# Kernel tuning notes

Measured on AMD Instinct MI355X. Metric: run time of the kernel, lower is better.

Reference implementation:

```python
import jax, jax.numpy as jnp
import numpy as np

IN_FEATURES = 4096
OUT_FEATURES = 4096
BANDWIDTH = min(IN_FEATURES, OUT_FEATURES) // 8  # 512, as in the torch default


def band_indices(n_out, n_in, bw):
    """Vectorized equivalent of BandMatrix.create_band_indices (COO row/col lists)."""
    i = np.arange(n_out)
    lo = np.maximum(0, i - bw)
    hi = np.minimum(n_in, i + bw + 1)
    counts = hi - lo
    total = int(counts.sum())
    rows = np.repeat(i, counts)
    start = np.cumsum(counts) - counts  # offset of each row's first entry
    cols = np.arange(total) - np.repeat(start, counts) + np.repeat(lo, counts)
    return rows.astype(np.int32), cols.astype(np.int32)


def setup_inputs() -> dict:
    key = jax.random.key(0)
    kx, kw = jax.random.split(key)
    rows_np, cols_np = band_indices(OUT_FEATURES, IN_FEATURES, BANDWIDTH)
    nnz = rows_np.shape[0]  # 3935744
    x = jax.random.normal(kx, (4, 2048, IN_FEATURES), dtype=jnp.float32)
    W_values = jax.random.normal(kw, (nnz,), dtype=jnp.float32)
    bias = jnp.zeros((OUT_FEATURES,), dtype=jnp.float32)
    return {
        "x": x,
        "W_values": W_values,
        "bias": bias,
        "rows": jnp.asarray(rows_np),
        "cols": jnp.asarray(cols_np),
    }


def reference(x, W_values, bias, rows, cols):
    # Densify banded COO weight [out, in] (matches sparse_coo_tensor().to_dense()).
    W = jnp.zeros((OUT_FEATURES, IN_FEATURES), dtype=W_values.dtype).at[rows, cols].set(W_values)
    # x: [B, S, in] @ W.T: [in, out] -> [B, S, out]
    out = jnp.einsum('bsi,oi->bso', x, W) + bias
    return out
```

## Files before the change

kernel.cpp:

```cpp
#include <hip/hip_runtime.h>
#include <stdint.h>

#define IN_F  4096
#define OUT_F 4096
#define BW    512
#define WB2   1280
#define BM    256
#define BN    256

typedef __bf16 bf16x8 __attribute__((ext_vector_type(8)));
typedef float  f32x4  __attribute__((ext_vector_type(4)));

__device__ __forceinline__ int band_start(int o) {
    if (o <= 512)  return o * 513 + ((o * (o - 1)) >> 1);
    if (o <= 3584) return 393472 + (o - 512) * 1025;
    const int d = o - 3584;
    return 3542272 + (((1024 + 4609 - o) * d) >> 1);
}

__device__ __forceinline__ uint16_t f32_to_bf16(float f) {
    uint32_t u = __builtin_bit_cast(uint32_t, f);
    u += 0x7FFFu + ((u >> 16) & 1u);
    return (uint16_t)(u >> 16);
}

__global__ __launch_bounds__(256) void cvt_x(const float* __restrict__ x,
                                             uint16_t* __restrict__ xb, int n4) {
    const int stride = gridDim.x * 256;
    for (int i = blockIdx.x * 256 + threadIdx.x; i < n4; i += stride) {
        const float4 v = reinterpret_cast<const float4*>(x)[i];
        const uint32_t lo = (uint32_t)f32_to_bf16(v.x) | ((uint32_t)f32_to_bf16(v.y) << 16);
        const uint32_t hi = (uint32_t)f32_to_bf16(v.z) | ((uint32_t)f32_to_bf16(v.w) << 16);
        reinterpret_cast<uint2*>(xb)[i] = make_uint2(lo, hi);
    }
}

__global__ __launch_bounds__(256) void cvt_w(const float* __restrict__ wv,
                                             uint16_t* __restrict__ wd) {
    const int o = blockIdx.y;
    const int j = blockIdx.x * 256 + threadIdx.x;
    const int i = (o & ~(BM - 1)) - BW + j;
    uint16_t v = 0;
    if (i >= o - BW && i <= o + BW && i >= 0 && i < IN_F) {
        const int lo = (o > BW) ? (o - BW) : 0;
        v = f32_to_bf16(wv[band_start(o) + (i - lo)]);
    }
    wd[o * WB2 + j] = v;
}

__global__ __launch_bounds__(512, 1) void band_gemm_v5(
    const uint16_t* __restrict__ xb,
    const uint16_t* __restrict__ wd,
    const float* __restrict__ bias,
    float* __restrict__ out)
{
    __shared__ __align__(128) uint8_t lds[131072];

    const int id  = blockIdx.x;
    const int xcd = id & 7;
    const int r   = id >> 3;
    const int bx  = 2 * xcd + (r & 1);
    const int by  = r >> 1;
    const int brow = by * BM;
    const int bcol = bx * BN;

    const int wlo    = bcol - BW;
    const int kstart = wlo > 0 ? wlo : 0;
    const int kend   = (bcol + BN + BW) < IN_F ? (bcol + BN + BW) : IN_F;
    const int nt     = (kend - kstart) >> 6;
    const int j0     = kstart - wlo;

    const int tid  = threadIdx.x;
    const int w    = tid >> 6;
    const int lane = tid & 63;
    const int ln   = lane & 15;
    const int kc   = lane >> 4;
    const int wm   = w >> 2;
    const int wn   = w & 3;

    const int srow = tid >> 3;
    const int csrc = (tid & 7) ^ (srow & 7);
    const uint16_t* aSrc = xb + (size_t)(brow + srow) * IN_F + kstart + csrc * 8;
    const uint16_t* bSrc = wd + (size_t)(bcol + srow) * WB2 + j0 + csrc * 8;

#define GLOAD(srcp, dst_off)                                                             \
    __builtin_amdgcn_global_load_lds(                                                    \
        (const __attribute__((address_space(1))) uint32_t*)(srcp),                       \
        (__attribute__((address_space(3))) uint32_t*)(lds + (dst_off) + (w << 10)),      \
        16, 0, 0)

#define STAGE(ts_, sb_) {                                                                \
        const uint16_t* as_ = aSrc + (ts_) * 64;                                         \
        const uint16_t* bs_ = bSrc + (ts_) * 64;                                         \
        GLOAD(as_,                        (sb_) + 0);                                    \
        GLOAD(as_ + (size_t)64  * IN_F,   (sb_) + 8192);                                 \
        GLOAD(as_ + (size_t)128 * IN_F,   (sb_) + 16384);                                \
        GLOAD(as_ + (size_t)192 * IN_F,   (sb_) + 24576);                                \
        GLOAD(bs_,                        (sb_) + 32768);                                 \
        GLOAD(bs_ + (size_t)64  * WB2,    (sb_) + 40960);                                \
        GLOAD(bs_ + (size_t)128 * WB2,    (sb_) + 49152);                                \
        GLOAD(bs_ + (size_t)192 * WB2,    (sb_) + 57344); }

    const int cswz = (kc ^ (ln & 7)) << 4;
    int aOff[8], bOff[4];
    #pragma unroll
    for (int a = 0; a < 8; ++a) aOff[a] = ((wm * 128 + a * 16 + ln) << 7) + cswz;
    #pragma unroll
    for (int n = 0; n < 4; ++n) bOff[n] = 32768 + ((wn * 64 + n * 16 + ln) << 7) + cswz;

    f32x4 acc[8][4] = {};

    STAGE(0, 0);
    asm volatile("s_waitcnt vmcnt(0)" ::: "memory");
    __builtin_amdgcn_s_barrier();

    for (int t = 0; t < nt; ++t) {
        const int cur = (t & 1) << 16;

        if (t + 1 < nt) STAGE(t + 1, cur ^ 65536);

        bf16x8 bfr[4][2];
        #pragma unroll
        for (int n = 0; n < 4; ++n) {
            bfr[n][0] = *(const bf16x8*)(lds + cur + bOff[n]);
            bfr[n][1] = *(const bf16x8*)(lds + cur + (bOff[n] ^ 64));
        }

        #pragma unroll
        for (int mq = 0; mq < 2; ++mq) {
            bf16x8 af[4][2];
            #pragma unroll
            for (int a = 0; a < 4; ++a) {
                af[a][0] = *(const bf16x8*)(lds + cur + aOff[mq * 4 + a]);
                af[a][1] = *(const bf16x8*)(lds + cur + (aOff[mq * 4 + a] ^ 64));
            }
            __builtin_amdgcn_s_setprio(1);
            #pragma unroll
            for (int a = 0; a < 4; ++a)
                #pragma unroll
                for (int n = 0; n < 4; ++n) {
                    acc[mq * 4 + a][n] = __builtin_amdgcn_mfma_f32_16x16x32_bf16(
                        af[a][0], bfr[n][0], acc[mq * 4 + a][n], 0, 0, 0);
                    acc[mq * 4 + a][n] = __builtin_amdgcn_mfma_f32_16x16x32_bf16(
                        af[a][1], bfr[n][1], acc[mq * 4 + a][n], 0, 0, 0);
                }
            __builtin_amdgcn_s_setprio(0);
        }

        asm volatile("s_waitcnt vmcnt(0)" ::: "memory");
        __builtin_amdgcn_s_barrier();
    }
#undef STAGE
#undef GLOAD

    const int ocol = bcol + wn * 64 + ln;
    float bsv[4];
    #pragma unroll
    for (int n = 0; n < 4; ++n) bsv[n] = bias[ocol + n * 16];

    #pragma unroll
    for (int a = 0; a < 8; ++a) {
        #pragma unroll
        for (int q = 0; q < 4; ++q) {
            const int row = brow + wm * 128 + a * 16 + (kc << 2) + q;
            float* po = out + (size_t)row * OUT_F + ocol;
            #pragma unroll
            for (int n = 0; n < 4; ++n)
                po[n * 16] = acc[a][n][q] + bsv[n];
        }
    }
}

__global__ __launch_bounds__(256) void band_gemm_f32(
    const float* __restrict__ x, const float* __restrict__ wv,
    const float* __restrict__ bias, float* __restrict__ out, int M)
{
    __shared__ float Xs[128][33];
    __shared__ float Ws[32][130];
    const int tid = threadIdx.x;
    const int tx = tid & 15, ty = tid >> 4;
    const int bcol = blockIdx.x * 128, brow = blockIdx.y * 128;
    const int klo = (bcol >= BW) ? (bcol - BW) : 0;
    const int khi = min(IN_F, bcol + 128 + BW);
    float acc[8][8];
    #pragma unroll
    for (int a = 0; a < 8; ++a)
        #pragma unroll
        for (int b = 0; b < 8; ++b) acc[a][b] = 0.f;
    const int xc4 = (tid & 7) * 4, xr0 = tid >> 3;
    const int wc = tid & 31, wr0 = tid >> 5;
    for (int k0 = klo; k0 < khi; k0 += 32) {
        #pragma unroll
        for (int p = 0; p < 4; ++p) {
            const int r = xr0 + 32 * p;
            const float4 v = *reinterpret_cast<const float4*>(&x[(size_t)(brow + r) * IN_F + (k0 + xc4)]);
            Xs[r][xc4 + 0] = v.x; Xs[r][xc4 + 1] = v.y; Xs[r][xc4 + 2] = v.z; Xs[r][xc4 + 3] = v.w;
        }
        const int i = k0 + wc;
        #pragma unroll
        for (int p = 0; p < 16; ++p) {
            const int rr = wr0 + 8 * p;
            const int o = bcol + rr;
            const int lo = (o >= BW) ? (o - BW) : 0;
            float v = 0.f;
            if (i >= o - BW && i <= o + BW) v = wv[band_start(o) + (i - lo)];
            Ws[wc][rr] = v;
        }
        __syncthreads();
        #pragma unroll
        for (int k = 0; k < 32; ++k) {
            float am[8];
            #pragma unroll
            for (int a = 0; a < 8; ++a) am[a] = Xs[ty * 8 + a][k];
            float bo[8];
            #pragma unroll
            for (int b = 0; b < 4; ++b) { bo[b] = Ws[k][tx * 4 + b]; bo[4 + b] = Ws[k][tx * 4 + 64 + b]; }
            #pragma unroll
            for (int a = 0; a < 8; ++a)
                #pragma unroll
                for (int b = 0; b < 8; ++b) acc[a][b] = fmaf(am[a], bo[b], acc[a][b]);
        }
        __syncthreads();
    }
    #pragma unroll
    for (int a = 0; a < 8; ++a) {
        const size_t row = (size_t)(brow + ty * 8 + a);
        #pragma unroll
        for (int b = 0; b < 4; ++b) {
            out[row * OUT_F + bcol + tx * 4 + b]      = acc[a][b]     + bias[bcol + tx * 4 + b];
            out[row * OUT_F + bcol + tx * 4 + 64 + b] = acc[a][4 + b] + bias[bcol + tx * 4 + 64 + b];
        }
    }
}

extern "C" void kernel_launch(void* const* d_in, const int* in_sizes, int n_in,
                              void* d_out, int out_size, void* d_ws, size_t ws_size,
                              hipStream_t stream) {
    const float* x    = (const float*)d_in[0];
    const float* wv   = (const float*)d_in[1];
    const float* bias = (const float*)d_in[2];
    float* out        = (float*)d_out;

    const int M = in_sizes[0] / IN_F;
    const size_t xb_bytes = (size_t)M * IN_F * 2;
    const size_t wd_bytes = (size_t)OUT_F * WB2 * 2;

    if (ws_size >= xb_bytes + wd_bytes && (M % BM) == 0) {
        uint16_t* xb  = (uint16_t*)d_ws;
        uint16_t* wdp = (uint16_t*)((uint8_t*)d_ws + xb_bytes);
        cvt_x<<<2048, 256, 0, stream>>>(x, xb, M * IN_F / 4);
        cvt_w<<<dim3(WB2 / 256, OUT_F), 256, 0, stream>>>(wv, wdp);
        band_gemm_v5<<<(M / BM) * (OUT_F / BN), 512, 0, stream>>>(xb, wdp, bias, out);
    } else {
        dim3 grid(OUT_F / 128, M / 128);
        band_gemm_f32<<<grid, 256, 0, stream>>>(x, wv, bias, out, M);
    }
}
```

Baseline: 140.7 us.

## Restructure band GEMM main loop into finer-grained phased load/compute pipeline

Replaces the simple double-buffered K loop with a two-tile-unrolled schedule. Each 64-wide K tile is split into A and B halves that are staged independently, interleaved with four MFMA quadrant phases, barriers, and partial vmcnt waits. This lets global-to-LDS loads overlap MFMA work more finely instead of waiting for all loads at the end of each iteration. Launch bounds also change to request 2 blocks per CU. The 128 KB LDS allocation likely keeps occupancy at one block, while the extra register pressure and barriers add risk. The loop assumes an even tile count.

After: 142.5 us. About the same (+1.3%).

```diff
diff --git a/kernel.cpp b/kernel.cpp
--- a/kernel.cpp
+++ b/kernel.cpp
@@ -48,7 +48,7 @@
     wd[o * WB2 + j] = v;
 }
 
-__global__ __launch_bounds__(512, 1) void band_gemm_v5(
+__global__ __launch_bounds__(512, 2) void band_gemm_v6(
     const uint16_t* __restrict__ xb,
     const uint16_t* __restrict__ wd,
     const float* __restrict__ bias,
@@ -68,6 +68,7 @@
     const int kstart = wlo > 0 ? wlo : 0;
     const int kend   = (bcol + BN + BW) < IN_F ? (bcol + BN + BW) : IN_F;
     const int nt     = (kend - kstart) >> 6;
+    const int niter  = nt >> 1;
     const int j0     = kstart - wlo;
 
     const int tid  = threadIdx.x;
@@ -89,68 +90,94 @@
         (__attribute__((address_space(3))) uint32_t*)(lds + (dst_off) + (w << 10)),      \
         16, 0, 0)
 
-#define STAGE(ts_, sb_) {                                                                \
-        const uint16_t* as_ = aSrc + (ts_) * 64;                                         \
-        const uint16_t* bs_ = bSrc + (ts_) * 64;                                         \
-        GLOAD(as_,                        (sb_) + 0);                                    \
-        GLOAD(as_ + (size_t)64  * IN_F,   (sb_) + 8192);                                 \
-        GLOAD(as_ + (size_t)128 * IN_F,   (sb_) + 16384);                                \
-        GLOAD(as_ + (size_t)192 * IN_F,   (sb_) + 24576);                                \
-        GLOAD(bs_,                        (sb_) + 32768);                                 \
-        GLOAD(bs_ + (size_t)64  * WB2,    (sb_) + 40960);                                \
-        GLOAD(bs_ + (size_t)128 * WB2,    (sb_) + 49152);                                \
-        GLOAD(bs_ + (size_t)192 * WB2,    (sb_) + 57344); }
-
-    const int cswz = (kc ^ (ln & 7)) << 4;
-    int aOff[8], bOff[4];
-    #pragma unroll
-    for (int a = 0; a < 8; ++a) aOff[a] = ((wm * 128 + a * 16 + ln) << 7) + cswz;
-    #pragma unroll
-    for (int n = 0; n < 4; ++n) bOff[n] = 32768 + ((wn * 64 + n * 16 + ln) << 7) + cswz;
+#define STG_A(v, h, dst) { const uint16_t* p_ = aSrc + (size_t)((h) * 128) * IN_F + (v) * 64; \
+        GLOAD(p_, dst); GLOAD(p_ + (size_t)64 * IN_F, (dst) + 8192); }
+#define STG_B(v, h, dst) { const uint16_t* p_ = bSrc + (size_t)((h) * 128) * WB2 + (v) * 64;  \
+        GLOAD(p_, dst); GLOAD(p_ + (size_t)64 * WB2, (dst) + 8192); }
+
+    const int cswz     = (kc ^ (ln & 7)) << 4;
+    const int aRowBase = wm * 16384 + (ln << 7);
+    const int bRowBase = (wn >> 1) * 16384 + (((wn & 1) * 64 + ln) << 7);
+
+#define LD_AF(BB, MQ) {                                                                  \
+    _Pragma("unroll")                                                                    \
+    for (int a_ = 0; a_ < 4; ++a_) {                                                     \
+        af[a_][0] = *(const bf16x8*)(lds + (BB) + aRowBase + (MQ) * 8192 + a_ * 2048 + cswz);        \
+        af[a_][1] = *(const bf16x8*)(lds + (BB) + aRowBase + (MQ) * 8192 + a_ * 2048 + (cswz ^ 64)); \
+    } }
+#define LD_BF(BB, NQ, BF) {                                                              \
+    _Pragma("unroll")                                                                    \
+    for (int n_ = 0; n_ < 2; ++n_) {                                                     \
+        BF[n_][0] = *(const bf16x8*)(lds + (BB) + bRowBase + (NQ) * 4096 + n_ * 2048 + cswz);        \
+        BF[n_][1] = *(const bf16x8*)(lds + (BB) + bRowBase + (NQ) * 4096 + n_ * 2048 + (cswz ^ 64)); \
+    } }
+#define MFMA16(MQ, NQ, BF) {                                                             \
+    _Pragma("unroll")                                                                    \
+    for (int a_ = 0; a_ < 4; ++a_) {                                                     \
+        _Pragma("unroll")                                                                \
+        for (int n_ = 0; n_ < 2; ++n_) {                                                 \
+            acc[(MQ)*4+a_][(NQ)*2+n_] = __builtin_amdgcn_mfma_f32_16x16x32_bf16(         \
+                af[a_][0], BF[n_][0], acc[(MQ)*4+a_][(NQ)*2+n_], 0, 0, 0);               \
+            acc[(MQ)*4+a_][(NQ)*2+n_] = __builtin_amdgcn_mfma_f32_16x16x32_bf16(         \
+                af[a_][1], BF[n_][1], acc[(MQ)*4+a_][(NQ)*2+n_], 0, 0, 0);               \
+        } } }
+#define PH_SYNC  __builtin_amdgcn_s_barrier();                                           \
+                 asm volatile("s_waitcnt lgkmcnt(0)" ::: "memory");                      \
+                 __builtin_amdgcn_sched_barrier(0);                                      \
+                 __builtin_amdgcn_s_setprio(1)
+#define PH_END   __builtin_amdgcn_s_setprio(0);                                          \
+                 __builtin_amdgcn_s_barrier()
 
     f32x4 acc[8][4] = {};
 
-    STAGE(0, 0);
-    asm volatile("s_waitcnt vmcnt(0)" ::: "memory");
+    STG_A(0, 0, 0);      STG_A(0, 1, 16384);
+    STG_B(0, 0, 32768);  STG_B(0, 1, 49152);
+    STG_B(1, 0, 98304);  STG_A(1, 0, 65536);
+    asm volatile("s_waitcnt vmcnt(4)" ::: "memory");
     __builtin_amdgcn_s_barrier();
 
-    for (int t = 0; t < nt; ++t) {
-        const int cur = (t & 1) << 16;
-
-        if (t + 1 < nt) STAGE(t + 1, cur ^ 65536);
-
-        bf16x8 bfr[4][2];
-        #pragma unroll
-        for (int n = 0; n < 4; ++n) {
-            bfr[n][0] = *(const bf16x8*)(lds + cur + bOff[n]);
-            bfr[n][1] = *(const bf16x8*)(lds + cur + (bOff[n] ^ 64));
-        }
-
-        #pragma unroll
-        for (int mq = 0; mq < 2; ++mq) {
-            bf16x8 af[4][2];
-            #pragma unroll
-            for (int a = 0; a < 4; ++a) {
-                af[a][0] = *(const bf16x8*)(lds + cur + aOff[mq * 4 + a]);
-                af[a][1] = *(const bf16x8*)(lds + cur + (aOff[mq * 4 + a] ^ 64));
-            }
-            __builtin_amdgcn_s_setprio(1);
-            #pragma unroll
-            for (int a = 0; a < 4; ++a)
-                #pragma unroll
-                for (int n = 0; n < 4; ++n) {
-                    acc[mq * 4 + a][n] = __builtin_amdgcn_mfma_f32_16x16x32_bf16(
-                        af[a][0], bfr[n][0], acc[mq * 4 + a][n], 0, 0, 0);
-                    acc[mq * 4 + a][n] = __builtin_amdgcn_mfma_f32_16x16x32_bf16(
-                        af[a][1], bfr[n][1], acc[mq * 4 + a][n], 0, 0, 0);
-                }
-            __builtin_amdgcn_s_setprio(0);
-        }
-
-        asm volatile("s_waitcnt vmcnt(0)" ::: "memory");
-        __builtin_amdgcn_s_barrier();
-    }
-#undef STAGE
+    for (int t = 0; t < niter; ++t) {
+        const int u   = 2 * t;
+        const bool st = (t + 1 < niter);
+        bf16x8 af[4][2], bf0[2][2], bf1[2][2];
+
+        LD_AF(0, 0); LD_BF(32768, 0, bf0);
+        STG_A(u + 1, 1, 81920);
+        PH_SYNC; MFMA16(0, 0, bf0); PH_END;
+        LD_BF(32768, 1, bf1);
+        STG_B(u + 1, 1, 114688);
+        PH_SYNC; MFMA16(0, 1, bf1); PH_END;
+        LD_AF(0, 1);
+        if (st) STG_B(u + 2, 0, 32768);
+        PH_SYNC; MFMA16(1, 1, bf1); PH_END;
+        if (st) STG_A(u + 2, 0, 0);
+        __builtin_amdgcn_s_barrier();
+        __builtin_amdgcn_s_setprio(1);
+        MFMA16(1, 0, bf0);
+        __builtin_amdgcn_s_setprio(0);
+        if (st) { asm volatile("s_waitcnt vmcnt(4)" ::: "memory"); }
+        else    { asm volatile("s_waitcnt vmcnt(0)" ::: "memory"); }
+        __builtin_amdgcn_s_barrier();
+        LD_AF(65536, 0); LD_BF(98304, 0, bf0);
+        if (st) STG_A(u + 2, 1, 16384);
+        PH_SYNC; MFMA16(0, 0, bf0); PH_END;
+        LD_BF(98304, 1, bf1);
+        if (st) STG_B(u + 2, 1, 49152);
+        PH_SYNC; MFMA16(0, 1, bf1); PH_END;
+        LD_AF(65536, 1);
+        if (st) STG_B(u + 3, 0, 98304);
+        PH_SYNC; MFMA16(1, 1, bf1); PH_END;
+        if (st) STG_A(u + 3, 0, 65536);
+        __builtin_amdgcn_s_barrier();
+        __builtin_amdgcn_s_setprio(1);
+        MFMA16(1, 0, bf0);
+        __builtin_amdgcn_s_setprio(0);
+        if (st) { asm volatile("s_waitcnt vmcnt(4)" ::: "memory"); }
+        else    { asm volatile("s_waitcnt vmcnt(0)" ::: "memory"); }
+        __builtin_amdgcn_s_barrier();
+    }
+#undef STG_A
+#undef STG_B
 #undef GLOAD
 
     const int ocol = bcol + wn * 64 + ln;
@@ -192,9 +219,9 @@
     for (int k0 = klo; k0 < khi; k0 += 32) {
         #pragma unroll
         for (int p = 0; p < 4; ++p) {
-            const int r = xr0 + 32 * p;
-            const float4 v = *reinterpret_cast<const float4*>(&x[(size_t)(brow + r) * IN_F + (k0 + xc4)]);
-            Xs[r][xc4 + 0] = v.x; Xs[r][xc4 + 1] = v.y; Xs[r][xc4 + 2] = v.z; Xs[r][xc4 + 3] = v.w;
+            const int rr = xr0 + 32 * p;
+            const float4 v = *reinterpret_cast<const float4*>(&x[(size_t)(brow + rr) * IN_F + (k0 + xc4)]);
+            Xs[rr][xc4 + 0] = v.x; Xs[rr][xc4 + 1] = v.y; Xs[rr][xc4 + 2] = v.z; Xs[rr][xc4 + 3] = v.w;
         }
         const int i = k0 + wc;
         #pragma unroll
@@ -250,7 +277,7 @@
         uint16_t* wdp = (uint16_t*)((uint8_t*)d_ws + xb_bytes);
         cvt_x<<<2048, 256, 0, stream>>>(x, xb, M * IN_F / 4);
         cvt_w<<<dim3(WB2 / 256, OUT_F), 256, 0, stream>>>(wv, wdp);
-        band_gemm_v5<<<(M / BM) * (OUT_F / BN), 512, 0, stream>>>(xb, wdp, bias, out);
+        band_gemm_v6<<<(M / BM) * (OUT_F / BN), 512, 0, stream>>>(xb, wdp, bias, out);
     } else {
         dim3 grid(OUT_F / 128, M / 128);
         band_gemm_f32<<<grid, 256, 0, stream>>>(x, wv, bias, out, M);
```

## Software-pipeline LDS fragment loads with MFMA quadrants and prefetch two stages ahead

Applied to the files above, without the earlier changes.

Restructures the main loop of the banded bf16 GEMM into a ping-pong schedule. LDS fragment loads for the next quadrant and next tile are interleaved with MFMA blocks, and global-to-LDS staging is issued two tiles ahead instead of one. The goal is to hide LDS read latency and global load latency behind matrix-core work. The cost is more live registers for the double fragment buffers, an extra barrier per iteration, and more intricate synchronisation that could introduce races if the vmcnt and barrier placement is wrong.

Result: no change. 143.1 us (+1.7%).

```diff
diff --git a/kernel.cpp b/kernel.cpp
--- a/kernel.cpp
+++ b/kernel.cpp
@@ -48,7 +48,7 @@
     wd[o * WB2 + j] = v;
 }
 
-__global__ __launch_bounds__(512, 1) void band_gemm_v5(
+__global__ __launch_bounds__(512, 1) void band_gemm_v7(
     const uint16_t* __restrict__ xb,
     const uint16_t* __restrict__ wd,
     const float* __restrict__ bias,
@@ -96,7 +96,7 @@
         GLOAD(as_ + (size_t)64  * IN_F,   (sb_) + 8192);                                 \
         GLOAD(as_ + (size_t)128 * IN_F,   (sb_) + 16384);                                \
         GLOAD(as_ + (size_t)192 * IN_F,   (sb_) + 24576);                                \
-        GLOAD(bs_,                        (sb_) + 32768);                                 \
+        GLOAD(bs_,                        (sb_) + 32768);                                \
         GLOAD(bs_ + (size_t)64  * WB2,    (sb_) + 40960);                                \
         GLOAD(bs_ + (size_t)128 * WB2,    (sb_) + 49152);                                \
         GLOAD(bs_ + (size_t)192 * WB2,    (sb_) + 57344); }
@@ -108,47 +108,62 @@
     #pragma unroll
     for (int n = 0; n < 4; ++n) bOff[n] = 32768 + ((wn * 64 + n * 16 + ln) << 7) + cswz;
 
+    bf16x8 a0[4][2], a1[4][2], b0[2][2], b1[2][2];
+
+#define LD_A(DST, BB, MQ) {                                                              \
+    _Pragma("unroll")                                                                    \
+    for (int a_ = 0; a_ < 4; ++a_) {                                                     \
+        DST[a_][0] = *(const bf16x8*)(lds + (BB) + aOff[(MQ) * 4 + a_]);                 \
+        DST[a_][1] = *(const bf16x8*)(lds + (BB) + (aOff[(MQ) * 4 + a_] ^ 64));          \
+    } }
+#define LD_B(DST, BB, NQ) {                                                              \
+    _Pragma("unroll")                                                                    \
+    for (int n_ = 0; n_ < 2; ++n_) {                                                     \
+        DST[n_][0] = *(const bf16x8*)(lds + (BB) + bOff[(NQ) * 2 + n_]);                 \
+        DST[n_][1] = *(const bf16x8*)(lds + (BB) + (bOff[(NQ) * 2 + n_] ^ 64));          \
+    } }
+#define MFMAQ(AF, BF, MQ, NQ) {                                                          \
+    __builtin_amdgcn_s_setprio(1);                                                       \
+    _Pragma("unroll")                                                                    \
+    for (int a_ = 0; a_ < 4; ++a_) {                                                     \
+        _Pragma("unroll")                                                                \
+        for (int n_ = 0; n_ < 2; ++n_) {                                                 \
+            acc[(MQ)*4+a_][(NQ)*2+n_] = __builtin_amdgcn_mfma_f32_16x16x32_bf16(         \
+                AF[a_][0], BF[n_][0], acc[(MQ)*4+a_][(NQ)*2+n_], 0, 0, 0);               \
+            acc[(MQ)*4+a_][(NQ)*2+n_] = __builtin_amdgcn_mfma_f32_16x16x32_bf16(         \
+                AF[a_][1], BF[n_][1], acc[(MQ)*4+a_][(NQ)*2+n_], 0, 0, 0);               \
+        } }                                                                              \
+    __builtin_amdgcn_s_setprio(0); }
+
     f32x4 acc[8][4] = {};
 
     STAGE(0, 0);
-    asm volatile("s_waitcnt vmcnt(0)" ::: "memory");
+    STAGE(1, 65536);
+    asm volatile("s_waitcnt vmcnt(8)" ::: "memory");
     __builtin_amdgcn_s_barrier();
-
-    for (int t = 0; t < nt; ++t) {
-        const int cur = (t & 1) << 16;
-
-        if (t + 1 < nt) STAGE(t + 1, cur ^ 65536);
-
-        bf16x8 bfr[4][2];
-        #pragma unroll
-        for (int n = 0; n < 4; ++n) {
-            bfr[n][0] = *(const bf16x8*)(lds + cur + bOff[n]);
-            bfr[n][1] = *(const bf16x8*)(lds + cur + (bOff[n] ^ 64));
-        }
-
-        #pragma unroll
-        for (int mq = 0; mq < 2; ++mq) {
-            bf16x8 af[4][2];
-            #pragma unroll
-            for (int a = 0; a < 4; ++a) {
-                af[a][0] = *(const bf16x8*)(lds + cur + aOff[mq * 4 + a]);
-                af[a][1] = *(const bf16x8*)(lds + cur + (aOff[mq * 4 + a] ^ 64));
-            }
-            __builtin_amdgcn_s_setprio(1);
-            #pragma unroll
-            for (int a = 0; a < 4; ++a)
-                #pragma unroll
-                for (int n = 0; n < 4; ++n) {
-                    acc[mq * 4 + a][n] = __builtin_amdgcn_mfma_f32_16x16x32_bf16(
-                        af[a][0], bfr[n][0], acc[mq * 4 + a][n], 0, 0, 0);
-                    acc[mq * 4 + a][n] = __builtin_amdgcn_mfma_f32_16x16x32_bf16(
-                        af[a][1], bfr[n][1], acc[mq * 4 + a][n], 0, 0, 0);
-                }
-            __builtin_amdgcn_s_setprio(0);
-        }
-
+    LD_A(a0, 0, 0);
+    LD_B(b1, 0, 1);
+
+    for (int v = 0; v < nt; ++v) {
+        const int cur = (v & 1) << 16;
+        const int nxt = cur ^ 65536;
+
+        LD_B(b0, cur, 0);
+        LD_A(a1, cur, 1);
+        MFMAQ(a0, b0, 0, 0);
+
+        MFMAQ(a0, b1, 0, 1);
         asm volatile("s_waitcnt vmcnt(0)" ::: "memory");
         __builtin_amdgcn_s_barrier();
+
+        if (v + 1 < nt) LD_A(a0, nxt, 0);
+        MFMAQ(a1, b1, 1, 1);
+        __builtin_amdgcn_s_barrier();
+        __builtin_amdgcn_sched_barrier(0);
+
+        if (v + 2 < nt) STAGE(v + 2, cur);
+        if (v + 1 < nt) LD_B(b1, nxt, 1);
+        MFMAQ(a1, b0, 1, 0);
     }
 #undef STAGE
 #undef GLOAD
@@ -192,9 +207,9 @@
     for (int k0 = klo; k0 < khi; k0 += 32) {
         #pragma unroll
         for (int p = 0; p < 4; ++p) {
-            const int r = xr0 + 32 * p;
-            const float4 v = *reinterpret_cast<const float4*>(&x[(size_t)(brow + r) * IN_F + (k0 + xc4)]);
-            Xs[r][xc4 + 0] = v.x; Xs[r][xc4 + 1] = v.y; Xs[r][xc4 + 2] = v.z; Xs[r][xc4 + 3] = v.w;
+            const int rr = xr0 + 32 * p;
+            const float4 v = *reinterpret_cast<const float4*>(&x[(size_t)(brow + rr) * IN_F + (k0 + xc4)]);
+            Xs[rr][xc4 + 0] = v.x; Xs[rr][xc4 + 1] = v.y; Xs[rr][xc4 + 2] = v.z; Xs[rr][xc4 + 3] = v.w;
         }
         const int i = k0 + wc;
         #pragma unroll
@@ -250,7 +265,7 @@
         uint16_t* wdp = (uint16_t*)((uint8_t*)d_ws + xb_bytes);
         cvt_x<<<2048, 256, 0, stream>>>(x, xb, M * IN_F / 4);
         cvt_w<<<dim3(WB2 / 256, OUT_F), 256, 0, stream>>>(wv, wdp);
-        band_gemm_v5<<<(M / BM) * (OUT_F / BN), 512, 0, stream>>>(xb, wdp, bias, out);
+        band_gemm_v7<<<(M / BM) * (OUT_F / BN), 512, 0, stream>>>(xb, wdp, bias, out);
     } else {
         dim3 grid(OUT_F / 128, M / 128);
         band_gemm_f32<<<grid, 256, 0, stream>>>(x, wv, bias, out, M);
```
